# Kernel optimization log

Hardware: AMD Instinct MI355X
Metric: run time of the kernel (lower is better)

The kernel has to match this reference:

```python
import jax, jax.numpy as jnp
import numpy as np

HEADS = 8

def _rotate_every_two(t):
    # t: [..., d]; interleaved rotation (-x2, x1) pairs
    x1 = t[..., ::2]
    x2 = t[..., 1::2]
    return jnp.stack([-x2, x1], axis=-1).reshape(t.shape)

def _theta_shift(t, sin, cos):
    return t * cos + _rotate_every_two(t) * sin

def setup_inputs() -> dict:
    key = jax.random.key(0)
    ks = jax.random.split(key, 5)
    B, H, W, C = 4, 40, 40, 512
    dh = C // HEADS
    x = jax.random.normal(ks[0], (B, H, W, C), dtype=jnp.float32)
    sin = jax.random.normal(ks[1], (H, W, dh), dtype=jnp.float32)
    cos = jax.random.normal(ks[2], (H, W, dh), dtype=jnp.float32)
    # 1x1 conv weight [3C, C] (kernel dims squeezed) + bias
    w_qkv = jax.random.normal(ks[3], (3 * C, C), dtype=jnp.float32) * (C ** -0.5)
    b_qkv = jnp.zeros((3 * C,), dtype=jnp.float32)
    return {"x": x, "sin": sin, "cos": cos, "w_qkv": w_qkv, "b_qkv": b_qkv}

def reference(x, sin, cos, w_qkv, b_qkv):
    B, H, W, C = x.shape
    heads = HEADS
    dh = C // heads
    scale = dh ** -0.5
    # 1x1 conv == per-pixel linear projection
    qkv = jnp.einsum('bhwc,oc->bhwo', x, w_qkv) + b_qkv  # [B,H,W,3C]
    q, k, v = jnp.split(qkv, 3, axis=-1)

    def to_heads(t):
        # channel order is (heads, dim_head) per the torch rearrange
        return t.reshape(B, H, W, heads, dh).transpose(0, 3, 1, 2, 4)  # [B,heads,H,W,dh]

    q = _theta_shift(to_heads(q), sin, cos)
    k = _theta_shift(to_heads(k), sin, cos)
    # v is computed but unused downstream in the original module (bug preserved)

    N = H * W
    q = q.reshape(B, heads, N, dh)
    k = k.reshape(B, heads, N, dh)

    attn = jnp.einsum('bhnd,bhmd->bhnm', q, k) * scale  # [B,heads,N,N]
    p = jax.nn.softmax(attn, axis=-1)
    # NOTE: original code does matmul(logist, kfine_heads) — K, not V. Kept faithful.
    out = jnp.einsum('bhnm,bhmd->bhnd', p, k)  # [B,heads,N,dh]
    out = out.transpose(0, 2, 1, 3).reshape(B, H, W, C)
    return out
```

## Files before the change

### kernel.cpp

```cpp
#include <hip/hip_runtime.h>
#include <hip/hip_bf16.h>


typedef __hip_bfloat16 bf16;
typedef __attribute__((ext_vector_type(8))) short short8;
typedef __attribute__((ext_vector_type(4))) short bfx4;
typedef __attribute__((ext_vector_type(4))) float f32x4;

#define NSP 1600
#define CDIM 512
#define DH 64

__device__ __forceinline__ f32x4 mfma32(short8 a, short8 b, f32x4 c) {
  return __builtin_amdgcn_mfma_f32_16x16x32_bf16(a, b, c, 0, 0, 0);
}

#if __has_builtin(__builtin_amdgcn_mfma_f32_16x16x16bf16_1k)
__device__ __forceinline__ f32x4 mfma_k16(bfx4 a, bfx4 b, f32x4 c) {
  return __builtin_amdgcn_mfma_f32_16x16x16bf16_1k(a, b, c, 0, 0, 0);
}
#else
__device__ __forceinline__ f32x4 mfma_k16(bfx4 a, bfx4 b, f32x4 c) {
  short8 a8 = {a.x, a.y, a.z, a.w, 0, 0, 0, 0};
  short8 b8 = {b.x, b.y, b.z, b.w, 0, 0, 0, 0};
  return __builtin_amdgcn_mfma_f32_16x16x32_bf16(a8, b8, c, 0, 0, 0);
}
#endif

__device__ __forceinline__ short8 cvt8(float4 v0, float4 v1) {
  short8 r; bf16* p = (bf16*)&r;
  p[0] = __float2bfloat16(v0.x); p[1] = __float2bfloat16(v0.y);
  p[2] = __float2bfloat16(v0.z); p[3] = __float2bfloat16(v0.w);
  p[4] = __float2bfloat16(v1.x); p[5] = __float2bfloat16(v1.y);
  p[6] = __float2bfloat16(v1.z); p[7] = __float2bfloat16(v1.w);
  return r;
}

extern "C" __global__ __launch_bounds__(256)
void cvt_kernel(const float* __restrict__ x, const float* __restrict__ w,
                const float* __restrict__ sin_t, const float* __restrict__ cos_t,
                bf16* __restrict__ x_bf, bf16* __restrict__ w_bf,
                float* __restrict__ sinT, float* __restrict__ cosT)
{
  __shared__ float t_lds[64][68];
  const int bid = blockIdx.x, tid = threadIdx.x;
  if (bid < 1600) {
    const size_t i = (size_t)bid * 2048 + tid * 8;
    float4 v0 = *(const float4*)(x + i);
    float4 v1 = *(const float4*)(x + i + 4);
    *(short8*)(x_bf + i) = cvt8(v0, v1);
  } else if (bid < 1856) {
    const size_t i = (size_t)(bid - 1600) * 2048 + tid * 8;
    float4 v0 = *(const float4*)(w + i);
    float4 v1 = *(const float4*)(w + i + 4);
    *(short8*)(w_bf + i) = cvt8(v0, v1);
  } else {
    const int t = bid - 1856;
    const float* src = (t < 25) ? sin_t : cos_t;
    float* dst = (t < 25) ? sinT : cosT;
    const int nt = (t < 25) ? t : t - 25;
    const int r = tid >> 2, c = (tid & 3) * 16;
#pragma unroll
    for (int j = 0; j < 4; ++j)
      *(float4*)&t_lds[r][c + j * 4] =
          *(const float4*)(src + (size_t)(nt * 64 + r) * 64 + c + j * 4);
    __syncthreads();
#pragma unroll
    for (int j4 = 0; j4 < 4; ++j4) {
      float4 o;
      o.x = t_lds[c + j4 * 4 + 0][r];
      o.y = t_lds[c + j4 * 4 + 1][r];
      o.z = t_lds[c + j4 * 4 + 2][r];
      o.w = t_lds[c + j4 * 4 + 3][r];
      *(float4*)(dst + (size_t)r * NSP + nt * 64 + c + j4 * 4) = o;
    }
  }
}

extern "C" __global__ __launch_bounds__(256)
void proj_kernel(const bf16* __restrict__ x_bf, const bf16* __restrict__ w_bf,
                 const float* __restrict__ bias, const float* __restrict__ sinT,
                 const float* __restrict__ cosT, bf16* __restrict__ q_ws,
                 bf16* __restrict__ k2_ws, bf16* __restrict__ kt2_ws)
{
  __shared__ __align__(16) char smem[36864];
  bf16 (*x_lds)[72] = (bf16(*)[72])smem;
  bf16 (*w_lds)[72] = (bf16(*)[72])(smem + 18432);
  bf16* ep = (bf16*)smem;

  const int tid  = threadIdx.x;
  const int wave = tid >> 6;
  const int lane = tid & 63;
  const int col  = lane & 15;
  const int quad = lane >> 4;
  const int wm = wave >> 1, wo = wave & 1;
  const int m0 = blockIdx.x * 128;
  const int o0 = blockIdx.y * 128;

  f32x4 acc[4][4];
#pragma unroll
  for (int i = 0; i < 4; ++i)
#pragma unroll
    for (int j = 0; j < 4; ++j) acc[i][j] = {0.f, 0.f, 0.f, 0.f};

  const int srow = tid >> 1;
  const int sch  = (tid & 1) * 32;

  for (int kt = 0; kt < 8; ++kt) {
    __syncthreads();
    {
      const bf16* xs = x_bf + (size_t)(m0 + srow) * CDIM + kt * 64 + sch;
      const bf16* ws = w_bf + (size_t)(o0 + srow) * CDIM + kt * 64 + sch;
#pragma unroll
      for (int j = 0; j < 4; ++j) {
        *(short8*)&x_lds[srow][sch + j * 8] = *(const short8*)(xs + j * 8);
        *(short8*)&w_lds[srow][sch + j * 8] = *(const short8*)(ws + j * 8);
      }
    }
    __syncthreads();
#pragma unroll
    for (int half = 0; half < 2; ++half) {
      short8 af[4], bfr[4];
#pragma unroll
      for (int mt = 0; mt < 4; ++mt)
        af[mt] = *(short8*)&x_lds[wm * 64 + mt * 16 + col][half * 32 + quad * 8];
#pragma unroll
      for (int ot = 0; ot < 4; ++ot)
        bfr[ot] = *(short8*)&w_lds[wo * 64 + ot * 16 + col][half * 32 + quad * 8];
#pragma unroll
      for (int mt = 0; mt < 4; ++mt)
#pragma unroll
        for (int ot = 0; ot < 4; ++ot)
          acc[mt][ot] = mfma32(af[mt], bfr[ot], acc[mt][ot]);
    }
  }

  __syncthreads();
  const int b_idx = (m0 + wm * 64) / NSP;
  const int n0w   = m0 + wm * 64 - b_idx * NSP;
  const bool isq  = (o0 < 512);
#pragma unroll
  for (int ot = 0; ot < 4; ++ot) {
    const int o_local = wo * 64 + ot * 16 + col;
    const int o_g = o0 + o_local;
    const float bv = bias[o_g];
    const int d = o_g & 63;
#pragma unroll
    for (int mt = 0; mt < 4; ++mt) {
      const int nl = mt * 16 + quad * 4;
      float t[4], rot[4];
#pragma unroll
      for (int r = 0; r < 4; ++r) t[r] = acc[mt][ot][r] + bv;
#pragma unroll
      for (int r = 0; r < 4; ++r) {
        float tp = __shfl_xor(t[r], 1, 64);
        rot[r] = (lane & 1) ? tp : -tp;
      }
      const float4 c4 = *(const float4*)(cosT + (size_t)d * NSP + n0w + nl);
      const float4 s4 = *(const float4*)(sinT + (size_t)d * NSP + n0w + nl);
      float res[4];
      res[0] = t[0] * c4.x + rot[0] * s4.x;
      res[1] = t[1] * c4.y + rot[1] * s4.y;
      res[2] = t[2] * c4.z + rot[2] * s4.z;
      res[3] = t[3] * c4.w + rot[3] * s4.w;
      if (isq) {
#pragma unroll
        for (int r = 0; r < 4; ++r) res[r] *= 0.1803368801111204f;
      }
      bfx4 pk; bf16* pp = (bf16*)&pk;
#pragma unroll
      for (int r = 0; r < 4; ++r) pp[r] = __float2bfloat16(res[r]);
      *(bfx4*)&ep[o_local * 132 + wm * 64 + nl] = pk;
    }
  }
  __syncthreads();

  if (isq) {
    const int m_l = tid >> 1, half = tid & 1;
    const int gm = m0 + m_l;
    const int bi = gm / NSP, n = gm - bi * NSP;
    const int h = (o0 >> 6) + half;
    bf16* base = q_ws + ((size_t)(bi * 8 + h) * NSP + n) * 64;
#pragma unroll
    for (int c = 0; c < 8; ++c) {
      short8 v; bf16* vp = (bf16*)&v;
#pragma unroll
      for (int j = 0; j < 8; ++j) vp[j] = ep[(half * 64 + c * 8 + j) * 132 + m_l];
      *(short8*)(base + c * 8) = v;
    }
  } else {
    const int h0 = (o0 - 512) >> 6;
#pragma unroll
    for (int it = 0; it < 8; ++it) {
      const int ci = it * 256 + tid;
      const int hh = ci >> 10, T = (ci >> 9) & 1, inner = ci & 511;
      const int ccol = inner & 15, cq = (inner >> 4) & 3;
      const int f = (inner >> 6) & 1, ti = (inner >> 7) & 1, kh2 = (inner >> 8) & 1;
      const int gmb = m0 + T * 64;
      const int bi = gmb / NSP, ktile = (gmb - bi * NSP) >> 6;
      const int m_l = T * 64 + (2 * kh2 + ti) * 16 + ccol;
      const int er0 = hh * 64 + (f * 4 + cq) * 8;
      short8 v; bf16* vp = (bf16*)&v;
#pragma unroll
      for (int j = 0; j < 8; ++j) vp[j] = ep[(er0 + j) * 132 + m_l];
      *(short8*)(k2_ws +
          (((size_t)(bi * 8 + h0 + hh) * 25 + ktile) * 512 + inner) * 8) = v;
    }
#pragma unroll
    for (int it = 0; it < 8; ++it) {
      const int ci = it * 256 + tid;
      const int hh = ci >> 10, T = (ci >> 9) & 1, inner = ci & 511;
      const int ccol = inner & 15, cq = (inner >> 4) & 3;
      const int dt = (inner >> 6) & 3, kh2 = (inner >> 8) & 1;
      const int gmb = m0 + T * 64;
      const int bi = gmb / NSP, ktile = (gmb - bi * NSP) >> 6;
      const bf16* eprow =
          ep + (hh * 64 + dt * 16 + ccol) * 132 + T * 64 + kh2 * 32 + cq * 4;
      short8 v;
      ((bfx4*)&v)[0] = *(const bfx4*)(eprow);
      ((bfx4*)&v)[1] = *(const bfx4*)(eprow + 16);
      *(short8*)(kt2_ws +
          (((size_t)(bi * 8 + h0 + hh) * 25 + ktile) * 512 + inner) * 8) = v;
    }
  }
}

extern "C" __global__ __launch_bounds__(256)
void attn_kernel(const bf16* __restrict__ q_ws, const bf16* __restrict__ k2_ws,
                 const bf16* __restrict__ kt2_ws, float* __restrict__ out)
{
  __shared__ float red[2][64][20];

  const int qt = blockIdx.x, bh = blockIdx.y;
  const int b = bh >> 3, h = bh & 7;
  const int tid  = threadIdx.x;
  const int wave = tid >> 6;
  const int lane = tid & 63;
  const int col  = lane & 15;
  const int quad = lane >> 4;
  const int qg = wave & 1, kh = wave >> 1;

  short8 qb0, qb1;
  {
    const bf16* qp =
        q_ws + ((size_t)bh * NSP + qt * 32 + qg * 16 + col) * 64;
    qb0 = *(const short8*)(qp + quad * 8);
    qb1 = *(const short8*)(qp + 32 + quad * 8);
  }

  f32x4 oacc[4];
#pragma unroll
  for (int i = 0; i < 4; ++i) oacc[i] = {0.f, 0.f, 0.f, 0.f};
  float l_part = 0.f;

  const bf16* k2b  = k2_ws  + (size_t)bh * 25 * 4096;
  const bf16* kt2b = kt2_ws + (size_t)bh * 25 * 4096;

  for (int kt = 0; kt < 25; ++kt) {
    const bf16* kc  = k2b  + kt * 4096;
    const bf16* kc2 = kt2b + kt * 4096;

    short8 kf00 = *(const short8*)(kc + (((kh * 2 + 0) * 2 + 0) * 64 + lane) * 8);
    short8 kf01 = *(const short8*)(kc + (((kh * 2 + 0) * 2 + 1) * 64 + lane) * 8);
    short8 kf10 = *(const short8*)(kc + (((kh * 2 + 1) * 2 + 0) * 64 + lane) * 8);
    short8 kf11 = *(const short8*)(kc + (((kh * 2 + 1) * 2 + 1) * 64 + lane) * 8);
    short8 ktf0 = *(const short8*)(kc2 + ((kh * 4 + 0) * 64 + lane) * 8);
    short8 ktf1 = *(const short8*)(kc2 + ((kh * 4 + 1) * 64 + lane) * 8);
    short8 ktf2 = *(const short8*)(kc2 + ((kh * 4 + 2) * 64 + lane) * 8);
    short8 ktf3 = *(const short8*)(kc2 + ((kh * 4 + 3) * 64 + lane) * 8);

    f32x4 s0 = {0.f, 0.f, 0.f, 0.f}, s1 = {0.f, 0.f, 0.f, 0.f};
    s0 = mfma32(kf00, qb0, s0); s0 = mfma32(kf01, qb1, s0);
    s1 = mfma32(kf10, qb0, s1); s1 = mfma32(kf11, qb1, s1);

    bfx4 p0, p1;
    {
      bf16* pp0 = (bf16*)&p0; bf16* pp1 = (bf16*)&p1;
#pragma unroll
      for (int r = 0; r < 4; ++r) {
        s0[r] = exp2f(s0[r]); s1[r] = exp2f(s1[r]);
      }
      l_part += s0[0] + s0[1] + s0[2] + s0[3] + s1[0] + s1[1] + s1[2] + s1[3];
#pragma unroll
      for (int r = 0; r < 4; ++r) {
        pp0[r] = __float2bfloat16(s0[r]);
        pp1[r] = __float2bfloat16(s1[r]);
      }
    }

    {
      bfx4 a0 = __builtin_shufflevector(ktf0, ktf0, 0, 1, 2, 3);
      bfx4 a0h = __builtin_shufflevector(ktf0, ktf0, 4, 5, 6, 7);
      bfx4 a1 = __builtin_shufflevector(ktf1, ktf1, 0, 1, 2, 3);
      bfx4 a1h = __builtin_shufflevector(ktf1, ktf1, 4, 5, 6, 7);
      bfx4 a2 = __builtin_shufflevector(ktf2, ktf2, 0, 1, 2, 3);
      bfx4 a2h = __builtin_shufflevector(ktf2, ktf2, 4, 5, 6, 7);
      bfx4 a3 = __builtin_shufflevector(ktf3, ktf3, 0, 1, 2, 3);
      bfx4 a3h = __builtin_shufflevector(ktf3, ktf3, 4, 5, 6, 7);
      oacc[0] = mfma_k16(a0,  p0, oacc[0]);
      oacc[0] = mfma_k16(a0h, p1, oacc[0]);
      oacc[1] = mfma_k16(a1,  p0, oacc[1]);
      oacc[1] = mfma_k16(a1h, p1, oacc[1]);
      oacc[2] = mfma_k16(a2,  p0, oacc[2]);
      oacc[2] = mfma_k16(a2h, p1, oacc[2]);
      oacc[3] = mfma_k16(a3,  p0, oacc[3]);
      oacc[3] = mfma_k16(a3h, p1, oacc[3]);
    }
  }

  l_part += __shfl_xor(l_part, 16, 64);
  l_part += __shfl_xor(l_part, 32, 64);

  if (wave >= 2) {
    float* dst = &red[wave - 2][lane][0];
#pragma unroll
    for (int dt = 0; dt < 4; ++dt)
      *(f32x4*)(dst + dt * 4) = oacc[dt];
    dst[16] = l_part;
  }
  __syncthreads();
  if (wave < 2) {
    const float* srcr = &red[wave][lane][0];
#pragma unroll
    for (int dt = 0; dt < 4; ++dt)
      oacc[dt] += *(const f32x4*)(srcr + dt * 4);
    const float inv = 1.f / (l_part + srcr[16]);
    const int qrow = qt * 32 + qg * 16 + col;
    float* ob = out + ((size_t)b * NSP + qrow) * CDIM + h * 64;
#pragma unroll
    for (int dt = 0; dt < 4; ++dt) {
      float4 v;
      v.x = oacc[dt][0] * inv; v.y = oacc[dt][1] * inv;
      v.z = oacc[dt][2] * inv; v.w = oacc[dt][3] * inv;
      *(float4*)(ob + dt * 16 + quad * 4) = v;
    }
  }
}

extern "C" void kernel_launch(void* const* d_in, const int* in_sizes, int n_in,
                              void* d_out, int out_size, void* d_ws, size_t ws_size,
                              hipStream_t stream) {
  const float* x     = (const float*)d_in[0];
  const float* sin_t = (const float*)d_in[1];
  const float* cos_t = (const float*)d_in[2];
  const float* w_qkv = (const float*)d_in[3];
  const float* b_qkv = (const float*)d_in[4];
  float* out = (float*)d_out;

  const size_t QK = (size_t)32 * NSP * DH;
  bf16* q_ws   = (bf16*)d_ws;
  bf16* k2_ws  = q_ws + QK;
  bf16* kt2_ws = k2_ws + QK;
  bf16* x_bf   = kt2_ws + QK;
  bf16* w_bf   = x_bf + (size_t)6400 * CDIM;
  float* sinT  = (float*)(w_bf + (size_t)1024 * CDIM);
  float* cosT  = sinT + (size_t)DH * NSP;

  cvt_kernel<<<1906, 256, 0, stream>>>(x, w_qkv, sin_t, cos_t, x_bf, w_bf, sinT, cosT);

  dim3 gproj(50, 8);
  proj_kernel<<<gproj, 256, 0, stream>>>(x_bf, w_bf, b_qkv, sinT, cosT,
                                         q_ws, k2_ws, kt2_ws);

  dim3 gattn(50, 32);
  attn_kernel<<<gattn, 256, 0, stream>>>(q_ws, k2_ws, kt2_ws, out);
}
```

Before: 148.5 us.

## Fuse fp32-to-bf16 conversion into projection loads and widen attention blocks

The separate conversion pass for x and w_qkv is removed. The projection kernel now reads fp32 directly and converts to bf16 while staging tiles into LDS, which saves writing and re-reading the bf16 copies plus some launch work. The attention kernel moves to 512-thread blocks covering 64 queries, so each loaded K tile is shared across more query waves. The cost is more global traffic per projection tile (fp32 loads are re-read by each of the 8 output-column blocks), and fewer attention blocks (800), which lowers the number of blocks in flight.

```diff
diff --git a/kernel.cpp b/kernel.cpp
--- a/kernel.cpp
+++ b/kernel.cpp
@@ -37,48 +37,33 @@
 }
 
 extern "C" __global__ __launch_bounds__(256)
-void cvt_kernel(const float* __restrict__ x, const float* __restrict__ w,
-                const float* __restrict__ sin_t, const float* __restrict__ cos_t,
-                bf16* __restrict__ x_bf, bf16* __restrict__ w_bf,
-                float* __restrict__ sinT, float* __restrict__ cosT)
+void sincos_kernel(const float* __restrict__ sin_t, const float* __restrict__ cos_t,
+                   float* __restrict__ sinT, float* __restrict__ cosT)
 {
   __shared__ float t_lds[64][68];
-  const int bid = blockIdx.x, tid = threadIdx.x;
-  if (bid < 1600) {
-    const size_t i = (size_t)bid * 2048 + tid * 8;
-    float4 v0 = *(const float4*)(x + i);
-    float4 v1 = *(const float4*)(x + i + 4);
-    *(short8*)(x_bf + i) = cvt8(v0, v1);
-  } else if (bid < 1856) {
-    const size_t i = (size_t)(bid - 1600) * 2048 + tid * 8;
-    float4 v0 = *(const float4*)(w + i);
-    float4 v1 = *(const float4*)(w + i + 4);
-    *(short8*)(w_bf + i) = cvt8(v0, v1);
-  } else {
-    const int t = bid - 1856;
-    const float* src = (t < 25) ? sin_t : cos_t;
-    float* dst = (t < 25) ? sinT : cosT;
-    const int nt = (t < 25) ? t : t - 25;
-    const int r = tid >> 2, c = (tid & 3) * 16;
-#pragma unroll
-    for (int j = 0; j < 4; ++j)
-      *(float4*)&t_lds[r][c + j * 4] =
-          *(const float4*)(src + (size_t)(nt * 64 + r) * 64 + c + j * 4);
-    __syncthreads();
-#pragma unroll
-    for (int j4 = 0; j4 < 4; ++j4) {
-      float4 o;
-      o.x = t_lds[c + j4 * 4 + 0][r];
-      o.y = t_lds[c + j4 * 4 + 1][r];
-      o.z = t_lds[c + j4 * 4 + 2][r];
-      o.w = t_lds[c + j4 * 4 + 3][r];
-      *(float4*)(dst + (size_t)r * NSP + nt * 64 + c + j4 * 4) = o;
-    }
+  const int t = blockIdx.x, tid = threadIdx.x;
+  const float* src = (t < 25) ? sin_t : cos_t;
+  float* dst = (t < 25) ? sinT : cosT;
+  const int nt = (t < 25) ? t : t - 25;
+  const int r = tid >> 2, c = (tid & 3) * 16;
+#pragma unroll
+  for (int j = 0; j < 4; ++j)
+    *(float4*)&t_lds[r][c + j * 4] =
+        *(const float4*)(src + (size_t)(nt * 64 + r) * 64 + c + j * 4);
+  __syncthreads();
+#pragma unroll
+  for (int j4 = 0; j4 < 4; ++j4) {
+    float4 o;
+    o.x = t_lds[c + j4 * 4 + 0][r];
+    o.y = t_lds[c + j4 * 4 + 1][r];
+    o.z = t_lds[c + j4 * 4 + 2][r];
+    o.w = t_lds[c + j4 * 4 + 3][r];
+    *(float4*)(dst + (size_t)r * NSP + nt * 64 + c + j4 * 4) = o;
   }
 }
 
 extern "C" __global__ __launch_bounds__(256)
-void proj_kernel(const bf16* __restrict__ x_bf, const bf16* __restrict__ w_bf,
+void proj_kernel(const float* __restrict__ x, const float* __restrict__ w,
                  const float* __restrict__ bias, const float* __restrict__ sinT,
                  const float* __restrict__ cosT, bf16* __restrict__ q_ws,
                  bf16* __restrict__ k2_ws, bf16* __restrict__ kt2_ws)
@@ -109,12 +94,16 @@
   for (int kt = 0; kt < 8; ++kt) {
     __syncthreads();
     {
-      const bf16* xs = x_bf + (size_t)(m0 + srow) * CDIM + kt * 64 + sch;
-      const bf16* ws = w_bf + (size_t)(o0 + srow) * CDIM + kt * 64 + sch;
+      const float* xs = x + (size_t)(m0 + srow) * CDIM + kt * 64 + sch;
+      const float* ws = w + (size_t)(o0 + srow) * CDIM + kt * 64 + sch;
 #pragma unroll
       for (int j = 0; j < 4; ++j) {
-        *(short8*)&x_lds[srow][sch + j * 8] = *(const short8*)(xs + j * 8);
-        *(short8*)&w_lds[srow][sch + j * 8] = *(const short8*)(ws + j * 8);
+        float4 a0 = *(const float4*)(xs + j * 8);
+        float4 a1 = *(const float4*)(xs + j * 8 + 4);
+        *(short8*)&x_lds[srow][sch + j * 8] = cvt8(a0, a1);
+        float4 b0 = *(const float4*)(ws + j * 8);
+        float4 b1 = *(const float4*)(ws + j * 8 + 4);
+        *(short8*)&w_lds[srow][sch + j * 8] = cvt8(b0, b1);
       }
     }
     __syncthreads();
@@ -225,11 +214,11 @@
   }
 }
 
-extern "C" __global__ __launch_bounds__(256)
+extern "C" __global__ __launch_bounds__(512)
 void attn_kernel(const bf16* __restrict__ q_ws, const bf16* __restrict__ k2_ws,
                  const bf16* __restrict__ kt2_ws, float* __restrict__ out)
 {
-  __shared__ float red[2][64][20];
+  __shared__ float red[4][64][20];
 
   const int qt = blockIdx.x, bh = blockIdx.y;
   const int b = bh >> 3, h = bh & 7;
@@ -238,12 +227,12 @@
   const int lane = tid & 63;
   const int col  = lane & 15;
   const int quad = lane >> 4;
-  const int qg = wave & 1, kh = wave >> 1;
+  const int qg = wave & 3, kh = wave >> 2;
 
   short8 qb0, qb1;
   {
     const bf16* qp =
-        q_ws + ((size_t)bh * NSP + qt * 32 + qg * 16 + col) * 64;
+        q_ws + ((size_t)bh * NSP + qt * 64 + qg * 16 + col) * 64;
     qb0 = *(const short8*)(qp + quad * 8);
     qb1 = *(const short8*)(qp + 32 + quad * 8);
   }
@@ -289,13 +278,13 @@
     }
 
     {
-      bfx4 a0 = __builtin_shufflevector(ktf0, ktf0, 0, 1, 2, 3);
+      bfx4 a0  = __builtin_shufflevector(ktf0, ktf0, 0, 1, 2, 3);
       bfx4 a0h = __builtin_shufflevector(ktf0, ktf0, 4, 5, 6, 7);
-      bfx4 a1 = __builtin_shufflevector(ktf1, ktf1, 0, 1, 2, 3);
+      bfx4 a1  = __builtin_shufflevector(ktf1, ktf1, 0, 1, 2, 3);
       bfx4 a1h = __builtin_shufflevector(ktf1, ktf1, 4, 5, 6, 7);
-      bfx4 a2 = __builtin_shufflevector(ktf2, ktf2, 0, 1, 2, 3);
+      bfx4 a2  = __builtin_shufflevector(ktf2, ktf2, 0, 1, 2, 3);
       bfx4 a2h = __builtin_shufflevector(ktf2, ktf2, 4, 5, 6, 7);
-      bfx4 a3 = __builtin_shufflevector(ktf3, ktf3, 0, 1, 2, 3);
+      bfx4 a3  = __builtin_shufflevector(ktf3, ktf3, 0, 1, 2, 3);
       bfx4 a3h = __builtin_shufflevector(ktf3, ktf3, 4, 5, 6, 7);
       oacc[0] = mfma_k16(a0,  p0, oacc[0]);
       oacc[0] = mfma_k16(a0h, p1, oacc[0]);
@@ -311,21 +300,21 @@
   l_part += __shfl_xor(l_part, 16, 64);
   l_part += __shfl_xor(l_part, 32, 64);
 
-  if (wave >= 2) {
-    float* dst = &red[wave - 2][lane][0];
+  if (wave >= 4) {
+    float* dst = &red[wave - 4][lane][0];
 #pragma unroll
     for (int dt = 0; dt < 4; ++dt)
       *(f32x4*)(dst + dt * 4) = oacc[dt];
     dst[16] = l_part;
   }
   __syncthreads();
-  if (wave < 2) {
-    const float* srcr = &red[wave][lane][0];
+  if (wave < 4) {
+    const float* srcr = &red[qg][lane][0];
 #pragma unroll
     for (int dt = 0; dt < 4; ++dt)
       oacc[dt] += *(const f32x4*)(srcr + dt * 4);
     const float inv = 1.f / (l_part + srcr[16]);
-    const int qrow = qt * 32 + qg * 16 + col;
+    const int qrow = qt * 64 + qg * 16 + col;
     float* ob = out + ((size_t)b * NSP + qrow) * CDIM + h * 64;
 #pragma unroll
     for (int dt = 0; dt < 4; ++dt) {
@@ -351,17 +340,15 @@
   bf16* q_ws   = (bf16*)d_ws;
   bf16* k2_ws  = q_ws + QK;
   bf16* kt2_ws = k2_ws + QK;
-  bf16* x_bf   = kt2_ws + QK;
-  bf16* w_bf   = x_bf + (size_t)6400 * CDIM;
-  float* sinT  = (float*)(w_bf + (size_t)1024 * CDIM);
+  float* sinT  = (float*)(kt2_ws + QK);
   float* cosT  = sinT + (size_t)DH * NSP;
 
-  cvt_kernel<<<1906, 256, 0, stream>>>(x, w_qkv, sin_t, cos_t, x_bf, w_bf, sinT, cosT);
+  sincos_kernel<<<50, 256, 0, stream>>>(sin_t, cos_t, sinT, cosT);
 
   dim3 gproj(50, 8);
-  proj_kernel<<<gproj, 256, 0, stream>>>(x_bf, w_bf, b_qkv, sinT, cosT,
+  proj_kernel<<<gproj, 256, 0, stream>>>(x, w_qkv, b_qkv, sinT, cosT,
                                          q_ws, k2_ws, kt2_ws);
 
-  dim3 gattn(50, 32);
-  attn_kernel<<<gattn, 256, 0, stream>>>(q_ws, k2_ws, kt2_ws, out);
-}
+  dim3 gattn(25, 32);
+  attn_kernel<<<gattn, 512, 0, stream>>>(q_ws, k2_ws, kt2_ws, out);
+}
```

New measurement: 176.7 us. 19.0% more time.
